# Kernel tuning notes

Hardware: AMD Instinct MI355X
Metric: run time of the kernel (lower is better)

The kernel has to match this reference:

```python
import jax, jax.numpy as jnp
import numpy as np

HIDDEN = 512
HEADS = 8
HEAD_DIM = HIDDEN // HEADS  # 64
NUM_FEATURES = 256
EPS = 1e-4


def _gaussian_orthogonal_random_matrix(num_rows, num_cols, scaling=0, seed=1234):
    """Blocks of orthogonal rows from QR of gaussian matrices, rescaled (FAVOR+)."""
    rng = np.random.default_rng(seed)
    blocks = []
    full_blocks = num_rows // num_cols
    for _ in range(full_blocks):
        q, _ = np.linalg.qr(rng.standard_normal((num_cols, num_cols)))
        blocks.append(q.T)
    rem = num_rows - full_blocks * num_cols
    if rem > 0:
        q, _ = np.linalg.qr(rng.standard_normal((num_cols, num_cols)))
        blocks.append(q.T[:rem])
    mat = np.concatenate(blocks, axis=0)  # [num_rows, num_cols]
    if scaling == 0:
        # row norms of a fresh gaussian matrix (chi-distributed multipliers)
        multiplier = np.linalg.norm(rng.standard_normal((num_rows, num_cols)), axis=1)
    else:
        multiplier = np.sqrt(num_cols) * np.ones(num_rows)
    return (multiplier[:, None] * mat).astype(np.float32)


def _split_heads(x, b):
    # [b, n, hidden] -> [b, h, n, head_dim]
    return x.reshape(b, -1, HEADS, HEAD_DIM).transpose(0, 2, 1, 3)


def _phi(data, proj):
    """Nonnegative softmax kernel feature map (FAVOR+).
    data: [b,h,n,d], proj: [m,d] -> [b,h,n,m]"""
    d = data.shape[-1]
    m = proj.shape[0]
    x = data * (d ** -0.25)
    dash = jnp.einsum('bhnd,md->bhnm', x, proj)
    diag = 0.5 * jnp.sum(x * x, axis=-1, keepdims=True)
    return (m ** -0.5) * jnp.exp(dash - diag) + EPS


def setup_inputs() -> dict:
    key = jax.random.key(0)
    ks = jax.random.split(key, 12)
    b, n = 2, 8192
    s = HIDDEN ** -0.5
    inp = {
        'query': jax.random.normal(ks[0], (b, n, HIDDEN), jnp.float32),
        'key':   jax.random.normal(ks[1], (b, n, HIDDEN), jnp.float32),
        'value': jax.random.normal(ks[2], (b, n, HIDDEN), jnp.float32),
        'WQ_w': jax.random.normal(ks[3], (HIDDEN, HIDDEN), jnp.float32) * s,
        'WQ_b': jnp.zeros((HIDDEN,), jnp.float32),
        'WK_w': jax.random.normal(ks[4], (HIDDEN, HIDDEN), jnp.float32) * s,
        'WK_b': jnp.zeros((HIDDEN,), jnp.float32),
        'WV_w': jax.random.normal(ks[5], (HIDDEN, HIDDEN), jnp.float32) * s,
        'WV_b': jnp.zeros((HIDDEN,), jnp.float32),
        'WO_w': jax.random.normal(ks[6], (HIDDEN, HIDDEN), jnp.float32) * s,
        'WO_b': jnp.zeros((HIDDEN,), jnp.float32),
        'proj': jnp.asarray(_gaussian_orthogonal_random_matrix(NUM_FEATURES, HEAD_DIM)),
    }
    return inp


def reference(query, key, value, WQ_w, WQ_b, WK_w, WK_b, WV_w, WV_b, WO_w, WO_b, proj):
    b = query.shape[0]
    # torch Linear: y = x @ W.T + b
    Q = _split_heads(jnp.einsum('bnd,ed->bne', query, WQ_w) + WQ_b, b)
    K = _split_heads(jnp.einsum('bnd,ed->bne', key,   WK_w) + WK_b, b)
    V = _split_heads(jnp.einsum('bnd,ed->bne', value, WV_w) + WV_b, b)

    Qp = _phi(Q, proj)  # [b,h,n,m]
    Kp = _phi(K, proj)  # [b,h,n,m]

    # denominator: Q' @ sum_n K'  -> [b,h,n,1]
    denom = jnp.einsum('bhnm,bhm->bhn', Qp, jnp.sum(Kp, axis=2))[..., None]
    # linear attention: Q' @ (K'^T V), O(n*m*d)
    ctx = jnp.einsum('bhnm,bhnd->bhmd', Kp, V)
    attn = jnp.einsum('bhnm,bhmd->bhnd', Qp, ctx) / denom

    # faithful to original: .view(batch, -1, hidden) directly on [b,h,n,d]
    attn = attn.reshape(b, -1, HIDDEN)
    return jnp.einsum('bnd,ed->bne', attn, WO_w) + WO_b
```

## Files before the change

kernel.cpp:

```cpp
#include <hip/hip_runtime.h>

typedef __attribute__((ext_vector_type(8))) _Float16 f16x8;
typedef __attribute__((ext_vector_type(4))) float f32x4;

#define S4 0.35355339059327373f

static __device__ __forceinline__ ushort f2h(float f) {
  return __builtin_bit_cast(ushort, (_Float16)f);
}

static __device__ __forceinline__ void gload16(const void* g, void* l) {
  __builtin_amdgcn_global_load_lds((const __attribute__((address_space(1))) void*)g,
                                   (__attribute__((address_space(3))) void*)l, 16, 0, 0);
}

static __device__ __forceinline__ void cvt_store8(ushort* dst, float4 a, float4 b) {
  f16x8 h;
  h[0] = (_Float16)a.x; h[1] = (_Float16)a.y; h[2] = (_Float16)a.z; h[3] = (_Float16)a.w;
  h[4] = (_Float16)b.x; h[5] = (_Float16)b.y; h[6] = (_Float16)b.z; h[7] = (_Float16)b.w;
  *(f16x8*)dst = h;
}

template<int BM, int BN, int WR, int WC, int EPI, int ZMODE, int DIAG, int AF32, int BF32>
__global__ __launch_bounds__(256) void gemm_bt(
    const void* __restrict__ Av, const void* __restrict__ Bv,
    const float* __restrict__ bias, ushort* __restrict__ Cb,
    float* __restrict__ Cf, const float* __restrict__ rv0,
    float* __restrict__ dg,
    int K, int ldA, int ldB, int ldC, int Mz,
    long sAz, long sBz, long sCz)
{
  constexpr int BK = 32;
  constexpr int WTM = BM / WR, WTN = BN / WC;
  constexpr int MI = WTM / 16, NI = WTN / 16;
  constexpr int LDSB = (BM + BN) * 64;

  __shared__ uint4 smem4[LDSB / 16];
  char* smem = (char*)smem4;
  ushort* As = (ushort*)smem;
  ushort* Bs = (ushort*)(smem + BM * 64);

  const int tid = threadIdx.x;
  const int l = tid & 63, w = tid >> 6;
  const int wr = w / WC, wc = w % WC;
  const int lr = l & 15, lk = l >> 4;
  const int tm = blockIdx.x * BM, tn = blockIdx.y * BN;
  const int z = blockIdx.z;

  const ushort* Ah = (const ushort*)Av;
  const ushort* Bh = (const ushort*)Bv;
  const float*  Af = (const float*)Av;
  const float*  Bf = (const float*)Bv;
  long aoff = 0, boff = 0;
  if (ZMODE == 0) { aoff = (long)z * sAz; boff = (long)z * sBz; }
  if (ZMODE == 1) { aoff = (long)(z >> 3) * sAz + (z & 7) * 64; boff = (long)z * sBz; }
  if (ZMODE == 2) { aoff = (long)z * sAz; boff = (long)(z >> 3) * sBz + (z & 7) * 64; }
  if (ZMODE == 3) {
    aoff = (long)(z & 15) * sAz + (long)(z >> 4) * 1024;
    boff = (long)(z & 15) * sBz + (long)(z >> 4) * 1024;
  }
  Ah += aoff; Bh += boff; Af += aoff; Bf += boff;
  const float* rv = (EPI == 1 || EPI == 6) ? (rv0 + (long)z * Mz) : nullptr;
  const long coff = (long)z * sCz;

  f32x4 acc[MI][NI];
#pragma unroll
  for (int i = 0; i < MI; ++i)
#pragma unroll
    for (int j = 0; j < NI; ++j) acc[i][j] = f32x4{0.f, 0.f, 0.f, 0.f};

  for (int k0 = 0; k0 < K; k0 += BK) {
    if constexpr (AF32) {
      const int ar = tid >> 1, ac = (tid & 1) * 16;
      const float* g = Af + (long)(tm + ar) * ldA + k0 + ac;
      float4 f0 = *(const float4*)(g);
      float4 f1 = *(const float4*)(g + 4);
      float4 f2 = *(const float4*)(g + 8);
      float4 f3 = *(const float4*)(g + 12);
      cvt_store8(As + ar * 32 + ac, f0, f1);
      cvt_store8(As + ar * 32 + ac + 8, f2, f3);
    } else {
      constexpr int AB = BM * 64;
#pragma unroll
      for (int s = 0; s < (AB + 4095) / 4096; ++s) {
        const int base = s * 4096 + w * 1024;
        if (base < AB) {
          const int idx = base + l * 16;
          gload16(Ah + (long)(tm + (idx >> 6)) * ldA + k0 + ((idx & 63) >> 1),
                  (char*)As + base);
        }
      }
    }
    if constexpr (BF32) {
      const int br = tid >> 1, bc = (tid & 1) * 16;
      const float* g = Bf + (long)(tn + br) * ldB + k0 + bc;
      float4 f0 = *(const float4*)(g);
      float4 f1 = *(const float4*)(g + 4);
      float4 f2 = *(const float4*)(g + 8);
      float4 f3 = *(const float4*)(g + 12);
      cvt_store8(Bs + br * 32 + bc, f0, f1);
      cvt_store8(Bs + br * 32 + bc + 8, f2, f3);
    } else {
      constexpr int BB = BN * 64;
#pragma unroll
      for (int s = 0; s < (BB + 4095) / 4096; ++s) {
        const int base = s * 4096 + w * 1024;
        if (base < BB) {
          const int idx = base + l * 16;
          gload16(Bh + (long)(tn + (idx >> 6)) * ldB + k0 + ((idx & 63) >> 1),
                  (char*)Bs + base);
        }
      }
    }
    __syncthreads();

    f16x8 af[MI], bfr[NI];
#pragma unroll
    for (int mi = 0; mi < MI; ++mi)
      af[mi] = *(const f16x8*)(As + (wr * WTM + mi * 16 + lr) * 32 + lk * 8);
#pragma unroll
    for (int ni = 0; ni < NI; ++ni)
      bfr[ni] = *(const f16x8*)(Bs + (wc * WTN + ni * 16 + lr) * 32 + lk * 8);
#pragma unroll
    for (int mi = 0; mi < MI; ++mi)
#pragma unroll
      for (int ni = 0; ni < NI; ++ni)
        acc[mi][ni] = __builtin_amdgcn_mfma_f32_16x16x32_f16(af[mi], bfr[ni], acc[mi][ni], 0, 0, 0);
    __syncthreads();
  }

#pragma unroll
  for (int mi = 0; mi < MI; ++mi) {
#pragma unroll
    for (int j = 0; j < 4; ++j) {
      const int row = tm + wr * WTM + mi * 16 + lk * 4 + j;
      float ds = 0.f;
      float dv = 1.f;
      if (EPI == 7) dv = __shfl(acc[mi][NI - 1][j], (l & 48), 64);
#pragma unroll
      for (int ni = 0; ni < NI; ++ni) {
        if (EPI == 7 && ni == NI - 1) continue;
        const int col = tn + wc * WTN + ni * 16 + lr;
        float v = acc[mi][ni][j];
        if (EPI == 0 || EPI == 3) v += bias[col];
        if (EPI == 4) v += bias[row];
        if (EPI == 1) v = 0.0625f * __expf(v - rv[row]) + 1e-4f;
        if (EPI == 6) v = 0.0625f * __expf(v - rv[col]) + 1e-4f;
        if (EPI == 7) v = v / dv;
        if (DIAG) ds += v * v;
        if (EPI == 4) {
          const int b = col >> 13, nn = col & 8191;
          const int h = row >> 6, d = row & 63;
          Cb[(long)(b * 8 + h) * 655360 + (long)d * 8192 + nn] = f2h(v);
        } else if (EPI == 3 || EPI == 5) {
          Cf[coff + (long)row * ldC + col] = v;
        } else {
          Cb[coff + (long)row * ldC + col] = f2h(v);
        }
      }
      if (DIAG) {
        ds += __shfl_xor(ds, 1, 64);
        ds += __shfl_xor(ds, 2, 64);
        ds += __shfl_xor(ds, 4, 64);
        ds += __shfl_xor(ds, 8, 64);
        if (lr == 0) {
          const int b = row >> 13, nn = row & 8191;
          const int head = (tn + wc * WTN) >> 6;
          dg[(long)(b * 8 + head) * 8192 + nn] = 0.0625f * ds;
        }
      }
    }
  }
}

__global__ void cvt_k(const float* __restrict__ in, ushort* __restrict__ out,
                      int n4, float scale) {
  int i = blockIdx.x * blockDim.x + threadIdx.x;
  if (i >= n4) return;
  float4 v = ((const float4*)in)[i];
  ushort4 o;
  o.x = f2h(v.x * scale); o.y = f2h(v.y * scale);
  o.z = f2h(v.z * scale); o.w = f2h(v.w * scale);
  ((ushort4*)out)[i] = o;
}

__global__ __launch_bounds__(256) void vtpad_k(ushort* __restrict__ Vt) {
  const int i = blockIdx.x * 256 + threadIdx.x;
  const int bh = i >> 14, rem = i & 16383, r = rem >> 10, n8 = rem & 1023;
  const unsigned val = (r == 0) ? 0x3C003C00u : 0u;
  uint4 u; u.x = val; u.y = val; u.z = val; u.w = val;
  *(uint4*)(Vt + (long)bh * 655360 + (long)(64 + r) * 8192 + n8 * 8) = u;
}

__global__ __launch_bounds__(256) void ctxred_k(const float* __restrict__ cp,
                                                ushort* __restrict__ ctxb) {
  const int idx = blockIdx.x * 256 + threadIdx.x;
  const int bh = idx / 20480, rem = idx % 20480;
  float a = 0.f;
#pragma unroll
  for (int kc = 0; kc < 8; ++kc) a += cp[(long)(kc * 16 + bh) * 20480 + rem];
  ctxb[idx] = f2h(a);
}

extern "C" void kernel_launch(void* const* d_in, const int* in_sizes, int n_in,
                              void* d_out, int out_size, void* d_ws, size_t ws_size,
                              hipStream_t stream) {
  (void)in_sizes; (void)n_in; (void)out_size; (void)ws_size;
  const float* q  = (const float*)d_in[0];
  const float* k  = (const float*)d_in[1];
  const float* v  = (const float*)d_in[2];
  const float* wq = (const float*)d_in[3];
  const float* bq = (const float*)d_in[4];
  const float* wk = (const float*)d_in[5];
  const float* bk = (const float*)d_in[6];
  const float* wv = (const float*)d_in[7];
  const float* bv = (const float*)d_in[8];
  const float* wo = (const float*)d_in[9];
  const float* bo = (const float*)d_in[10];
  const float* pj = (const float*)d_in[11];

  char* ws = (char*)d_ws;
  ushort* attnR = (ushort*)(ws + 0);
  float*  cpart = (float*)(ws + 16777216);
  ushort* wqh   = (ushort*)(ws + 27262976);
  ushort* wkh   = (ushort*)(ws + 27787264);
  ushort* wvh   = (ushort*)(ws + 28311552);
  ushort* woh   = (ushort*)(ws + 28835840);
  ushort* pjh   = (ushort*)(ws + 29360128);
  ushort* Qh    = (ushort*)(ws + 29392896);
  ushort* Kh    = (ushort*)(ws + 46170112);
  ushort* Vt    = (ushort*)(ws + 62947328);
  ushort* Pbuf  = (ushort*)(ws + 83918848);
  float*  diagQ = (float*)(ws + 151027712);
  float*  diagK = (float*)(ws + 151552000);
  ushort* ctxb  = (ushort*)(ws + 152076288);

  cvt_k<<<256, 256, 0, stream>>>(wq, wqh, 65536, 1.f);
  cvt_k<<<256, 256, 0, stream>>>(wk, wkh, 65536, 1.f);
  cvt_k<<<256, 256, 0, stream>>>(wv, wvh, 65536, 1.f);
  cvt_k<<<256, 256, 0, stream>>>(wo, woh, 65536, 1.f);
  cvt_k<<<16, 256, 0, stream>>>(pj, pjh, 4096, S4);
  vtpad_k<<<1024, 256, 0, stream>>>(Vt);

  gemm_bt<128,128,2,2,0,0,1,1,0><<<dim3(128,4,1), 256, 0, stream>>>(
      q, wqh, bq, Qh, nullptr, nullptr, diagQ, 512, 512, 512, 512, 0, 0L, 0L, 0L);
  gemm_bt<128,128,2,2,0,0,1,1,0><<<dim3(128,4,1), 256, 0, stream>>>(
      k, wkh, bk, Kh, nullptr, nullptr, diagK, 512, 512, 512, 512, 0, 0L, 0L, 0L);

  gemm_bt<128,128,2,2,4,0,0,0,1><<<dim3(4,128,1), 256, 0, stream>>>(
      wvh, v, bv, Vt, nullptr, nullptr, nullptr, 512, 512, 512, 0, 0, 0L, 0L, 0L);

  gemm_bt<128,128,2,2,6,2,0,0,0><<<dim3(2,64,16), 256, 0, stream>>>(
      pjh, Kh, nullptr, Pbuf, nullptr, diagK, nullptr, 64, 64, 512, 8192, 8192,
      0L, 4194304L, 2097152L);

  gemm_bt<80,128,1,4,5,3,0,0,0><<<dim3(1,2,128), 256, 0, stream>>>(
      Vt, Pbuf, nullptr, nullptr, cpart, nullptr, nullptr, 1024, 8192, 8192, 256, 0,
      655360L, 2097152L, 20480L);
  ctxred_k<<<1280, 256, 0, stream>>>(cpart, ctxb);

  gemm_bt<128,128,2,2,1,1,0,0,0><<<dim3(64,2,16), 256, 0, stream>>>(
      Qh, pjh, nullptr, Pbuf, nullptr, diagQ, nullptr, 64, 512, 64, 256, 8192,
      4194304L, 0L, 2097152L);

  gemm_bt<128,80,4,1,7,0,0,0,0><<<dim3(64,1,16), 256, 0, stream>>>(
      Pbuf, ctxb, nullptr, attnR, nullptr, nullptr, nullptr, 256, 256, 256, 64, 8192,
      2097152L, 20480L, 524288L);

  gemm_bt<128,128,2,2,3,0,0,0,0><<<dim3(128,4,1), 256, 0, stream>>>(
      attnR, woh, bo, nullptr, (float*)d_out, nullptr, nullptr, 512, 512, 512, 512, 0,
      0L, 0L, 0L);
}
```

Before: 201.4 us.

## Fuse phi feature maps into context and attention GEMMs, dropping Pbuf round-trip

Replaces the separate phi(K) GEMM plus K'^T V GEMM with one kernel that computes phi(K) tiles in LDS and accumulates the context directly. It likewise fuses phi(Q) with the Q'·ctx GEMM and the denominator division into one kernel. This removes writing and rereading the large fp16 Pbuf feature buffer in global memory and cuts two launches. In exchange, the new kernels use ad hoc tiling with little double buffering, heavy LDS use (about 126KB in phiattn_k), and fewer blocks, so occupancy and latency hiding may suffer.

```diff
diff --git a/kernel.cpp b/kernel.cpp
--- a/kernel.cpp
+++ b/kernel.cpp
@@ -54,13 +54,8 @@
   long aoff = 0, boff = 0;
   if (ZMODE == 0) { aoff = (long)z * sAz; boff = (long)z * sBz; }
   if (ZMODE == 1) { aoff = (long)(z >> 3) * sAz + (z & 7) * 64; boff = (long)z * sBz; }
-  if (ZMODE == 2) { aoff = (long)z * sAz; boff = (long)(z >> 3) * sBz + (z & 7) * 64; }
-  if (ZMODE == 3) {
-    aoff = (long)(z & 15) * sAz + (long)(z >> 4) * 1024;
-    boff = (long)(z & 15) * sBz + (long)(z >> 4) * 1024;
-  }
   Ah += aoff; Bh += boff; Af += aoff; Bf += boff;
-  const float* rv = (EPI == 1 || EPI == 6) ? (rv0 + (long)z * Mz) : nullptr;
+  const float* rv = (EPI == 1) ? (rv0 + (long)z * Mz) : nullptr;
   const long coff = (long)z * sCz;
 
   f32x4 acc[MI][NI];
@@ -135,24 +130,19 @@
     for (int j = 0; j < 4; ++j) {
       const int row = tm + wr * WTM + mi * 16 + lk * 4 + j;
       float ds = 0.f;
-      float dv = 1.f;
-      if (EPI == 7) dv = __shfl(acc[mi][NI - 1][j], (l & 48), 64);
 #pragma unroll
       for (int ni = 0; ni < NI; ++ni) {
-        if (EPI == 7 && ni == NI - 1) continue;
         const int col = tn + wc * WTN + ni * 16 + lr;
         float v = acc[mi][ni][j];
         if (EPI == 0 || EPI == 3) v += bias[col];
         if (EPI == 4) v += bias[row];
         if (EPI == 1) v = 0.0625f * __expf(v - rv[row]) + 1e-4f;
-        if (EPI == 6) v = 0.0625f * __expf(v - rv[col]) + 1e-4f;
-        if (EPI == 7) v = v / dv;
         if (DIAG) ds += v * v;
         if (EPI == 4) {
           const int b = col >> 13, nn = col & 8191;
           const int h = row >> 6, d = row & 63;
           Cb[(long)(b * 8 + h) * 655360 + (long)d * 8192 + nn] = f2h(v);
-        } else if (EPI == 3 || EPI == 5) {
+        } else if (EPI == 3) {
           Cf[coff + (long)row * ldC + col] = v;
         } else {
           Cb[coff + (long)row * ldC + col] = f2h(v);
@@ -171,6 +161,236 @@
       }
     }
   }
+}
+
+__global__ __launch_bounds__(256) void phictx_k(
+    const ushort* __restrict__ Kh, const ushort* __restrict__ Vt,
+    const ushort* __restrict__ pjh, const float* __restrict__ diagK,
+    float* __restrict__ cpart)
+{
+  const int by = blockIdx.x, z = blockIdx.y;
+  const int kc = z >> 4, bh = z & 15;
+  const int b = bh >> 3, h = bh & 7;
+  const int n0c = kc * 1024;
+  const int tid = threadIdx.x, l = tid & 63, w = tid >> 6;
+  const int lr = l & 15, lk = l >> 4;
+
+  __shared__ char smem[39680];
+  ushort* Pj = (ushort*)smem;
+  ushort* Ks = (ushort*)(smem + 18432);
+  ushort* Vs = (ushort*)(smem + 23040);
+  ushort* Kp = (ushort*)(smem + 29440);
+
+  {
+    const ushort* src = pjh + by * 128 * 64;
+#pragma unroll
+    for (int c = tid; c < 1024; c += 256) {
+      const int row = c >> 3, cole = (c & 7) * 8;
+      *(uint4*)(Pj + row * 72 + cole) = *(const uint4*)(src + row * 64 + cole);
+    }
+  }
+  const ushort* KB = Kh + (long)b * 4194304 + h * 64;
+  const ushort* VB = Vt + (long)bh * 655360;
+  const float* rv = diagK + (long)bh * 8192;
+
+  f32x4 acc[5][2];
+#pragma unroll
+  for (int i = 0; i < 5; ++i) {
+    acc[i][0] = f32x4{0.f, 0.f, 0.f, 0.f};
+    acc[i][1] = f32x4{0.f, 0.f, 0.f, 0.f};
+  }
+
+  for (int ns = 0; ns < 32; ++ns) {
+    const int n0 = n0c + ns * 32;
+    {
+      const int row = tid >> 3, cole = (tid & 7) * 8;
+      uint4 u = *(const uint4*)(KB + (long)(n0 + row) * 512 + cole);
+      *(uint4*)(Ks + row * 72 + cole) = u;
+    }
+    {
+#pragma unroll
+      for (int c = tid; c < 320; c += 256) {
+        const int row = c >> 2, cole = (c & 3) * 8;
+        uint4 u = *(const uint4*)(VB + (long)row * 8192 + n0 + cole);
+        *(uint4*)(Vs + row * 40 + cole) = u;
+      }
+    }
+    __syncthreads();
+
+    f32x4 a2[2][2];
+    a2[0][0] = f32x4{0.f,0.f,0.f,0.f}; a2[0][1] = f32x4{0.f,0.f,0.f,0.f};
+    a2[1][0] = f32x4{0.f,0.f,0.f,0.f}; a2[1][1] = f32x4{0.f,0.f,0.f,0.f};
+#pragma unroll
+    for (int kk = 0; kk < 2; ++kk) {
+      f16x8 pa[2], kb[2];
+#pragma unroll
+      for (int mi = 0; mi < 2; ++mi)
+        pa[mi] = *(const f16x8*)(Pj + (w * 32 + mi * 16 + lr) * 72 + kk * 32 + lk * 8);
+#pragma unroll
+      for (int ni = 0; ni < 2; ++ni)
+        kb[ni] = *(const f16x8*)(Ks + (ni * 16 + lr) * 72 + kk * 32 + lk * 8);
+#pragma unroll
+      for (int mi = 0; mi < 2; ++mi)
+#pragma unroll
+        for (int ni = 0; ni < 2; ++ni)
+          a2[mi][ni] = __builtin_amdgcn_mfma_f32_16x16x32_f16(pa[mi], kb[ni], a2[mi][ni], 0, 0, 0);
+    }
+#pragma unroll
+    for (int mi = 0; mi < 2; ++mi)
+#pragma unroll
+      for (int ni = 0; ni < 2; ++ni)
+#pragma unroll
+        for (int j = 0; j < 4; ++j) {
+          const int mrow = w * 32 + mi * 16 + lk * 4 + j;
+          const int ncol = ni * 16 + lr;
+          const float vv = 0.0625f * __expf(a2[mi][ni][j] - rv[n0 + ncol]) + 1e-4f;
+          Kp[mrow * 40 + ncol] = f2h(vv);
+        }
+    __syncthreads();
+
+    f16x8 va[5], kb2[2];
+#pragma unroll
+    for (int mi = 0; mi < 5; ++mi)
+      va[mi] = *(const f16x8*)(Vs + (mi * 16 + lr) * 40 + lk * 8);
+#pragma unroll
+    for (int ni = 0; ni < 2; ++ni)
+      kb2[ni] = *(const f16x8*)(Kp + (w * 32 + ni * 16 + lr) * 40 + lk * 8);
+#pragma unroll
+    for (int mi = 0; mi < 5; ++mi)
+#pragma unroll
+      for (int ni = 0; ni < 2; ++ni)
+        acc[mi][ni] = __builtin_amdgcn_mfma_f32_16x16x32_f16(va[mi], kb2[ni], acc[mi][ni], 0, 0, 0);
+    __syncthreads();
+  }
+
+  float* out = cpart + (long)z * 20480;
+#pragma unroll
+  for (int mi = 0; mi < 5; ++mi)
+#pragma unroll
+    for (int ni = 0; ni < 2; ++ni)
+#pragma unroll
+      for (int j = 0; j < 4; ++j) {
+        const int row = mi * 16 + lk * 4 + j;
+        const int col = by * 128 + w * 32 + ni * 16 + lr;
+        out[(long)row * 256 + col] = acc[mi][ni][j];
+      }
+}
+
+__global__ __launch_bounds__(256) void phiattn_k(
+    const ushort* __restrict__ Qh, const ushort* __restrict__ pjh,
+    const float* __restrict__ diagQ, const ushort* __restrict__ ctxb,
+    ushort* __restrict__ attnR)
+{
+  const int bx = blockIdx.x, bh = blockIdx.y;
+  const int b = bh >> 3, h = bh & 7;
+  const int tm = bx * 128;
+  const int tid = threadIdx.x, l = tid & 63, w = tid >> 6;
+  const int lr = l & 15, lk = l >> 4;
+  const int wr = w >> 1, wc = w & 1;
+
+  __shared__ char smem[126208];
+  ushort* P  = (ushort*)smem;
+  ushort* Cs = (ushort*)(smem + 67584);
+  ushort* As = (ushort*)(smem + 109824);
+  ushort* Bs = (ushort*)(smem + 118016);
+
+  {
+    const ushort* cb = ctxb + (long)bh * 20480;
+#pragma unroll
+    for (int c = tid; c < 2560; c += 256) {
+      const int row = c >> 5, cole = (c & 31) * 8;
+      *(uint4*)(Cs + row * 264 + cole) = *(const uint4*)(cb + row * 256 + cole);
+    }
+  }
+  const ushort* QB = Qh + (long)b * 4194304 + h * 64;
+  const float* rv = diagQ + (long)bh * 8192;
+
+  for (int nh = 0; nh < 2; ++nh) {
+    const ushort* PB = pjh + nh * 8192;
+    f32x4 a2[4][4];
+#pragma unroll
+    for (int i = 0; i < 4; ++i)
+#pragma unroll
+      for (int j = 0; j < 4; ++j) a2[i][j] = f32x4{0.f, 0.f, 0.f, 0.f};
+
+    for (int k0 = 0; k0 < 64; k0 += 32) {
+#pragma unroll
+      for (int s = 0; s < 2; ++s) {
+        const int base = s * 4096 + w * 1024;
+        const int idx = base + l * 16;
+        gload16(QB + (long)(tm + (idx >> 6)) * 512 + k0 + ((idx & 63) >> 1),
+                (char*)As + base);
+      }
+#pragma unroll
+      for (int s = 0; s < 2; ++s) {
+        const int base = s * 4096 + w * 1024;
+        const int idx = base + l * 16;
+        gload16(PB + (long)(idx >> 6) * 64 + k0 + ((idx & 63) >> 1),
+                (char*)Bs + base);
+      }
+      __syncthreads();
+      f16x8 af[4], bfr[4];
+#pragma unroll
+      for (int mi = 0; mi < 4; ++mi)
+        af[mi] = *(const f16x8*)(As + (wr * 64 + mi * 16 + lr) * 32 + lk * 8);
+#pragma unroll
+      for (int ni = 0; ni < 4; ++ni)
+        bfr[ni] = *(const f16x8*)(Bs + (wc * 64 + ni * 16 + lr) * 32 + lk * 8);
+#pragma unroll
+      for (int mi = 0; mi < 4; ++mi)
+#pragma unroll
+        for (int ni = 0; ni < 4; ++ni)
+          a2[mi][ni] = __builtin_amdgcn_mfma_f32_16x16x32_f16(af[mi], bfr[ni], a2[mi][ni], 0, 0, 0);
+      __syncthreads();
+    }
+#pragma unroll
+    for (int mi = 0; mi < 4; ++mi)
+#pragma unroll
+      for (int ni = 0; ni < 4; ++ni)
+#pragma unroll
+        for (int j = 0; j < 4; ++j) {
+          const int row = wr * 64 + mi * 16 + lk * 4 + j;
+          const int col = nh * 128 + wc * 64 + ni * 16 + lr;
+          const float vv = 0.0625f * __expf(a2[mi][ni][j] - rv[tm + row]) + 1e-4f;
+          P[row * 264 + col] = f2h(vv);
+        }
+  }
+  __syncthreads();
+
+  f32x4 acc[2][5];
+#pragma unroll
+  for (int i = 0; i < 2; ++i)
+#pragma unroll
+    for (int j = 0; j < 5; ++j) acc[i][j] = f32x4{0.f, 0.f, 0.f, 0.f};
+
+  for (int k0 = 0; k0 < 256; k0 += 32) {
+    f16x8 pa[2], cbf[5];
+#pragma unroll
+    for (int mi = 0; mi < 2; ++mi)
+      pa[mi] = *(const f16x8*)(P + (w * 32 + mi * 16 + lr) * 264 + k0 + lk * 8);
+#pragma unroll
+    for (int ni = 0; ni < 5; ++ni)
+      cbf[ni] = *(const f16x8*)(Cs + (ni * 16 + lr) * 264 + k0 + lk * 8);
+#pragma unroll
+    for (int mi = 0; mi < 2; ++mi)
+#pragma unroll
+      for (int ni = 0; ni < 5; ++ni)
+        acc[mi][ni] = __builtin_amdgcn_mfma_f32_16x16x32_f16(pa[mi], cbf[ni], acc[mi][ni], 0, 0, 0);
+  }
+
+  ushort* outb = attnR + (long)bh * 524288;
+#pragma unroll
+  for (int mi = 0; mi < 2; ++mi)
+#pragma unroll
+    for (int j = 0; j < 4; ++j) {
+      const float dv = __shfl(acc[mi][4][j], (l & 48), 64);
+      const int row = tm + w * 32 + mi * 16 + lk * 4 + j;
+#pragma unroll
+      for (int ni = 0; ni < 4; ++ni) {
+        const int col = ni * 16 + lr;
+        outb[(long)row * 64 + col] = f2h(acc[mi][ni][j] / dv);
+      }
+    }
 }
 
 __global__ void cvt_k(const float* __restrict__ in, ushort* __restrict__ out,
@@ -230,10 +450,9 @@
   ushort* Qh    = (ushort*)(ws + 29392896);
   ushort* Kh    = (ushort*)(ws + 46170112);
   ushort* Vt    = (ushort*)(ws + 62947328);
-  ushort* Pbuf  = (ushort*)(ws + 83918848);
-  float*  diagQ = (float*)(ws + 151027712);
-  float*  diagK = (float*)(ws + 151552000);
-  ushort* ctxb  = (ushort*)(ws + 152076288);
+  float*  diagQ = (float*)(ws + 83918848);
+  float*  diagK = (float*)(ws + 84443136);
+  ushort* ctxb  = (ushort*)(ws + 84967424);
 
   cvt_k<<<256, 256, 0, stream>>>(wq, wqh, 65536, 1.f);
   cvt_k<<<256, 256, 0, stream>>>(wk, wkh, 65536, 1.f);
@@ -250,22 +469,10 @@
   gemm_bt<128,128,2,2,4,0,0,0,1><<<dim3(4,128,1), 256, 0, stream>>>(
       wvh, v, bv, Vt, nullptr, nullptr, nullptr, 512, 512, 512, 0, 0, 0L, 0L, 0L);
 
-  gemm_bt<128,128,2,2,6,2,0,0,0><<<dim3(2,64,16), 256, 0, stream>>>(
-      pjh, Kh, nullptr, Pbuf, nullptr, diagK, nullptr, 64, 64, 512, 8192, 8192,
-      0L, 4194304L, 2097152L);
-
-  gemm_bt<80,128,1,4,5,3,0,0,0><<<dim3(1,2,128), 256, 0, stream>>>(
-      Vt, Pbuf, nullptr, nullptr, cpart, nullptr, nullptr, 1024, 8192, 8192, 256, 0,
-      655360L, 2097152L, 20480L);
+  phictx_k<<<dim3(2,128), 256, 0, stream>>>(Kh, Vt, pjh, diagK, cpart);
   ctxred_k<<<1280, 256, 0, stream>>>(cpart, ctxb);
 
-  gemm_bt<128,128,2,2,1,1,0,0,0><<<dim3(64,2,16), 256, 0, stream>>>(
-      Qh, pjh, nullptr, Pbuf, nullptr, diagQ, nullptr, 64, 512, 64, 256, 8192,
-      4194304L, 0L, 2097152L);
-
-  gemm_bt<128,80,4,1,7,0,0,0,0><<<dim3(64,1,16), 256, 0, stream>>>(
-      Pbuf, ctxb, nullptr, attnR, nullptr, nullptr, nullptr, 256, 256, 256, 64, 8192,
-      2097152L, 20480L, 524288L);
+  phiattn_k<<<dim3(64,16), 256, 0, stream>>>(Qh, pjh, diagQ, ctxb, attnR);
 
   gemm_bt<128,128,2,2,3,0,0,0,0><<<dim3(128,4,1), 256, 0, stream>>>(
       attnR, woh, bo, nullptr, (float*)d_out, nullptr, nullptr, 512, 512, 512, 512, 0,
```

Result: slower. 210.0 us (+4.3%).
